# Optimization experiments

Measured on AMD Instinct MI355X. Metric: run time of the kernel, lower is better.

Reference implementation:

```python
import jax, jax.numpy as jnp
import numpy as np

FEATURE_DIM = 6272
UNITS = 32
B, L = 8, 256

def setup_inputs() -> dict:
    key = jax.random.key(0)
    k1, k2, k3, k4, k5 = jax.random.split(key, 5)
    return {
        "inputs": jax.random.normal(k1, (B, L, FEATURE_DIM), dtype=jnp.float32),
        "Wt": jax.random.normal(k2, (FEATURE_DIM, UNITS), dtype=jnp.float32) * 0.02,
        "bh": jax.random.normal(k3, (UNITS,), dtype=jnp.float32),
        "Wa": jax.random.normal(k4, (UNITS, 1), dtype=jnp.float32) * 0.02,
        "ba": jax.random.normal(k5, (1,), dtype=jnp.float32),
    }

def reference(inputs, Wt, bh, Wa, ba):
    # q == k: both projected through Wt (original code reuses Wt for both)
    p = jnp.einsum('blf,fu->blu', inputs, Wt)            # [B, L, U]
    # additive (Bahdanau-style) pairwise combine: [B, L, L, U]
    beta = jnp.tanh(p[:, :, None, :] + p[:, None, :, :] + bh)
    alpha = jnp.einsum('bqku,uo->bqk', beta, Wa) + ba[0]  # [B, L, L]
    alpha = jax.nn.sigmoid(alpha)
    a = jax.nn.softmax(alpha, axis=-1)                    # softmax over keys
    c_r = jnp.einsum('bqk,bkf->bqf', a, inputs)           # [B, L, F]
    return c_r
```

## Files before the change

### kernel.cpp

```cpp
#include <hip/hip_runtime.h>
#include <hip/hip_bf16.h>
#include <math.h>

#define FDIM 6272
#define LQ   256
#define BN   8
#define UDIM 32
#define BL   (BN*LQ)

typedef short  short8 __attribute__((ext_vector_type(8)));
typedef float  f32x4  __attribute__((ext_vector_type(4)));

static __device__ __forceinline__ ushort f2bf(float f) {
    __hip_bfloat16 h = __float2bfloat16(f);
    return *(ushort*)&h;
}

__global__ __launch_bounds__(256)
void k_wtt(const float* __restrict__ Wt, ushort* __restrict__ wtt,
           float* __restrict__ pb) {
    const int gid = blockIdx.x * 256 + threadIdx.x;
    const int u = gid / 784, fg = gid % 784;
    ushort v[8];
    #pragma unroll
    for (int j = 0; j < 8; ++j)
        v[j] = f2bf(Wt[(size_t)(8 * fg + j) * UDIM + u]);
    *(uint4*)(wtt + (size_t)u * FDIM + 8 * fg) = *(uint4*)v;

    if (gid < BL * UDIM / 4)
        ((float4*)pb)[gid] = make_float4(0.f, 0.f, 0.f, 0.f);
}

__global__ __launch_bounds__(256)
void k1_mfma(const float* __restrict__ x, const ushort* __restrict__ wtt,
             float* __restrict__ pb) {
    __shared__ ushort As[32 * 40];
    __shared__ ushort Bs[32 * 40];

    const int t    = threadIdx.x;
    const int row0 = blockIdx.x * 32;
    const int f0   = blockIdx.y * 896;
    const int wv   = t >> 6, lane = t & 63;
    const int n16  = lane & 15, quad = lane >> 4;
    const int m0   = 16 * (wv & 1), n0 = 16 * (wv >> 1);

    const int srow = t >> 3, sg = t & 7;

    f32x4 acc = (f32x4){0.f, 0.f, 0.f, 0.f};

    for (int c = 0; c < 28; ++c) {
        const int kk = f0 + c * 32;
        __syncthreads();
        const float4 xv = *(const float4*)(x + (size_t)(row0 + srow) * FDIM + kk + 4 * sg);
        uint2 pk;
        pk.x = (unsigned)f2bf(xv.x) | ((unsigned)f2bf(xv.y) << 16);
        pk.y = (unsigned)f2bf(xv.z) | ((unsigned)f2bf(xv.w) << 16);
        *(uint2*)(As + srow * 40 + 4 * sg) = pk;
        *(uint2*)(Bs + srow * 40 + 4 * sg) =
            *(const uint2*)(wtt + (size_t)srow * FDIM + kk + 4 * sg);
        __syncthreads();

        const short8 af = *(const short8*)(As + (m0 + n16) * 40 + quad * 8);
        const short8 bf = *(const short8*)(Bs + (n0 + n16) * 40 + quad * 8);
        acc = __builtin_amdgcn_mfma_f32_16x16x32_bf16(af, bf, acc, 0, 0, 0);
    }

    #pragma unroll
    for (int r = 0; r < 4; ++r)
        atomicAdd(&pb[(size_t)(row0 + m0 + quad * 4 + r) * UDIM + n0 + n16], acc[r]);
}

__global__ __launch_bounds__(256)
void k2_attn(const float* __restrict__ pb, const float* __restrict__ bh,
             const float* __restrict__ Wa, const float* __restrict__ ba,
             ushort* __restrict__ ab) {
    const int bq = blockIdx.x;
    const int b  = bq >> 8;
    const int k  = threadIdx.x;

    __shared__ float pq_s[UDIM];
    __shared__ float wa_s[UDIM];
    __shared__ float pk_s[LQ * 33];
    __shared__ float red[4];

    if (k < UDIM) {
        pq_s[k] = pb[bq * UDIM + k] + bh[k];
        wa_s[k] = Wa[k];
    }
    const float* pbb = pb + (size_t)b * LQ * UDIM;
    #pragma unroll
    for (int i = 0; i < 32; ++i) {
        int idx = k + i * 256;
        pk_s[(idx >> 5) * 33 + (idx & 31)] = pbb[idx];
    }
    __syncthreads();

    const float* pk = &pk_s[k * 33];
    float s = 0.f;
    #pragma unroll
    for (int u = 0; u < UDIM; ++u)
        s = fmaf(tanhf(pq_s[u] + pk[u]), wa_s[u], s);

    const float alpha = 1.f / (1.f + expf(-(s + ba[0])));
    const float e = expf(alpha);

    float v = e;
    #pragma unroll
    for (int m = 1; m < 64; m <<= 1) v += __shfl_xor(v, m, 64);
    if ((k & 63) == 0) red[k >> 6] = v;
    __syncthreads();
    const float tot = red[0] + red[1] + red[2] + red[3];

    ab[(size_t)bq * LQ + k] = f2bf(e / tot);
}

__global__ __launch_bounds__(256, 3)
void k3_fused(const float* __restrict__ x, const ushort* __restrict__ ab,
              float* __restrict__ out) {
    __shared__ ushort Bs[64 * 40];

    const int t    = threadIdx.x;
    const int f0   = blockIdx.x * 64;
    const int b    = blockIdx.y;
    const int wv   = t >> 6;
    const int lane = t & 63;
    const int n16  = lane & 15;
    const int quad = lane >> 4;

    const int g  = t >> 4;
    const int kp = t & 15;

    const float*  xb  = x  + (size_t)b * LQ * FDIM + f0 + 4 * g;
    const ushort* abb = ab + (size_t)b * LQ * LQ;

    f32x4 acc[4][4];
    #pragma unroll
    for (int mf = 0; mf < 4; ++mf)
        #pragma unroll
        for (int nf = 0; nf < 4; ++nf)
            acc[mf][nf] = (f32x4){0.f, 0.f, 0.f, 0.f};

    for (int c = 0; c < 8; ++c) {
        const int kc = c * 32;
        __syncthreads();
        {
            const float4 v0 = *(const float4*)(xb + (size_t)(kc + 2 * kp    ) * FDIM);
            const float4 v1 = *(const float4*)(xb + (size_t)(kc + 2 * kp + 1) * FDIM);
            unsigned* bw = (unsigned*)Bs;
            bw[(4 * g + 0) * 20 + kp] = (unsigned)f2bf(v0.x) | ((unsigned)f2bf(v1.x) << 16);
            bw[(4 * g + 1) * 20 + kp] = (unsigned)f2bf(v0.y) | ((unsigned)f2bf(v1.y) << 16);
            bw[(4 * g + 2) * 20 + kp] = (unsigned)f2bf(v0.z) | ((unsigned)f2bf(v1.z) << 16);
            bw[(4 * g + 3) * 20 + kp] = (unsigned)f2bf(v0.w) | ((unsigned)f2bf(v1.w) << 16);
        }
        __syncthreads();

        short8 af[4];
        #pragma unroll
        for (int mf = 0; mf < 4; ++mf)
            af[mf] = *(const short8*)(abb + (size_t)(64 * wv + 16 * mf + n16) * LQ
                                      + kc + quad * 8);
        #pragma unroll
        for (int nf = 0; nf < 4; ++nf) {
            const short8 bf = *(const short8*)(Bs + (16 * nf + n16) * 40 + quad * 8);
            #pragma unroll
            for (int mf = 0; mf < 4; ++mf)
                acc[mf][nf] = __builtin_amdgcn_mfma_f32_16x16x32_bf16(af[mf], bf, acc[mf][nf], 0, 0, 0);
        }
    }

    float* ob = out + ((size_t)b * LQ + 64 * wv + quad * 4) * FDIM + f0 + n16;
    #pragma unroll
    for (int mf = 0; mf < 4; ++mf)
        #pragma unroll
        for (int nf = 0; nf < 4; ++nf)
            #pragma unroll
            for (int r = 0; r < 4; ++r)
                ob[(size_t)(16 * mf + r) * FDIM + 16 * nf] = acc[mf][nf][r];
}

extern "C" void kernel_launch(void* const* d_in, const int* in_sizes, int n_in,
                              void* d_out, int out_size, void* d_ws, size_t ws_size,
                              hipStream_t stream) {
    const float* x  = (const float*)d_in[0];
    const float* Wt = (const float*)d_in[1];
    const float* bh = (const float*)d_in[2];
    const float* Wa = (const float*)d_in[3];
    const float* ba = (const float*)d_in[4];
    float* out = (float*)d_out;

    float*  pb  = (float*)d_ws;
    ushort* ab  = (ushort*)((char*)d_ws + 262144);
    ushort* wtt = (ushort*)((char*)d_ws + 262144 + 1048576);

    k_wtt<<<98, 256, 0, stream>>>(Wt, wtt, pb);
    k1_mfma<<<dim3(64, 7), 256, 0, stream>>>(x, wtt, pb);
    k2_attn<<<BL, 256, 0, stream>>>(pb, bh, Wa, ba, ab);
    k3_fused<<<dim3(98, 8), 256, 0, stream>>>(x, ab, out);
}
```

Measured before the change: 168.5 us.

## Double-buffer k3 LDS tiles, drop LDS staging in k1, use fast math in k2

k3 now stages 64-deep K chunks into two LDS buffers, prefetching the next chunk's x into registers while the current chunk's MFMAs run. This halves the number of barriers and hides global load latency. k1 drops its shared-memory staging and loads MFMA fragments straight from global memory with an unrolled loop. k2 replaces tanhf, expf and division with raw v_exp/v_rcp approximations, which slightly reduces accuracy. k3 also loses its occupancy hint, and the larger LDS and register footprint may lower occupancy.

```diff
diff --git a/kernel.cpp b/kernel.cpp
--- a/kernel.cpp
+++ b/kernel.cpp
@@ -15,6 +15,22 @@
     __hip_bfloat16 h = __float2bfloat16(f);
     return *(ushort*)&h;
 }
+static __device__ __forceinline__ unsigned pk2(float a, float b) {
+    return (unsigned)f2bf(a) | ((unsigned)f2bf(b) << 16);
+}
+static __device__ __forceinline__ float fexp2(float x) {
+    float r;
+    asm volatile("v_exp_f32 %0, %1 \n s_nop 1" : "=v"(r) : "v"(x));
+    return r;
+}
+static __device__ __forceinline__ float frcp(float x) {
+    float r;
+    asm volatile("v_rcp_f32 %0, %1 \n s_nop 1" : "=v"(r) : "v"(x));
+    return r;
+}
+static __device__ __forceinline__ float tanh_fast(float v) {
+    return 1.f - 2.f * frcp(1.f + fexp2(v * 2.88539008177793f));
+}
 
 __global__ __launch_bounds__(256)
 void k_wtt(const float* __restrict__ Wt, ushort* __restrict__ wtt,
@@ -34,40 +50,34 @@
 __global__ __launch_bounds__(256)
 void k1_mfma(const float* __restrict__ x, const ushort* __restrict__ wtt,
              float* __restrict__ pb) {
-    __shared__ ushort As[32 * 40];
-    __shared__ ushort Bs[32 * 40];
-
     const int t    = threadIdx.x;
-    const int row0 = blockIdx.x * 32;
-    const int f0   = blockIdx.y * 896;
     const int wv   = t >> 6, lane = t & 63;
     const int n16  = lane & 15, quad = lane >> 4;
-    const int m0   = 16 * (wv & 1), n0 = 16 * (wv >> 1);
-
-    const int srow = t >> 3, sg = t & 7;
+    const int row0 = blockIdx.x * 32 + 16 * (wv & 1);
+    const int u0   = 16 * (wv >> 1);
+    const int f0   = blockIdx.y * 896;
+
+    const float*  xr = x   + (size_t)(row0 + n16) * FDIM + f0 + quad * 8;
+    const ushort* wr = wtt + (size_t)(u0   + n16) * FDIM + f0 + quad * 8;
 
     f32x4 acc = (f32x4){0.f, 0.f, 0.f, 0.f};
 
+    #pragma unroll 4
     for (int c = 0; c < 28; ++c) {
-        const int kk = f0 + c * 32;
-        __syncthreads();
-        const float4 xv = *(const float4*)(x + (size_t)(row0 + srow) * FDIM + kk + 4 * sg);
-        uint2 pk;
-        pk.x = (unsigned)f2bf(xv.x) | ((unsigned)f2bf(xv.y) << 16);
-        pk.y = (unsigned)f2bf(xv.z) | ((unsigned)f2bf(xv.w) << 16);
-        *(uint2*)(As + srow * 40 + 4 * sg) = pk;
-        *(uint2*)(Bs + srow * 40 + 4 * sg) =
-            *(const uint2*)(wtt + (size_t)srow * FDIM + kk + 4 * sg);
-        __syncthreads();
-
-        const short8 af = *(const short8*)(As + (m0 + n16) * 40 + quad * 8);
-        const short8 bf = *(const short8*)(Bs + (n0 + n16) * 40 + quad * 8);
+        const float4 a0 = *(const float4*)(xr + c * 32);
+        const float4 a1 = *(const float4*)(xr + c * 32 + 4);
+        short8 af;
+        af[0] = (short)f2bf(a0.x); af[1] = (short)f2bf(a0.y);
+        af[2] = (short)f2bf(a0.z); af[3] = (short)f2bf(a0.w);
+        af[4] = (short)f2bf(a1.x); af[5] = (short)f2bf(a1.y);
+        af[6] = (short)f2bf(a1.z); af[7] = (short)f2bf(a1.w);
+        const short8 bf = *(const short8*)(wr + c * 32);
         acc = __builtin_amdgcn_mfma_f32_16x16x32_bf16(af, bf, acc, 0, 0, 0);
     }
 
     #pragma unroll
     for (int r = 0; r < 4; ++r)
-        atomicAdd(&pb[(size_t)(row0 + m0 + quad * 4 + r) * UDIM + n0 + n16], acc[r]);
+        atomicAdd(&pb[(size_t)(row0 + quad * 4 + r) * UDIM + u0 + n16], acc[r]);
 }
 
 __global__ __launch_bounds__(256)
@@ -75,18 +85,15 @@
              const float* __restrict__ Wa, const float* __restrict__ ba,
              ushort* __restrict__ ab) {
     const int bq = blockIdx.x;
-    const int b  = bq >> 8;
+    const int b  = bq >> 8, q = bq & 255;
     const int k  = threadIdx.x;
 
+    __shared__ float pk_s[LQ * 33];
     __shared__ float pq_s[UDIM];
     __shared__ float wa_s[UDIM];
-    __shared__ float pk_s[LQ * 33];
     __shared__ float red[4];
 
-    if (k < UDIM) {
-        pq_s[k] = pb[bq * UDIM + k] + bh[k];
-        wa_s[k] = Wa[k];
-    }
+    if (k < UDIM) wa_s[k] = Wa[k];
     const float* pbb = pb + (size_t)b * LQ * UDIM;
     #pragma unroll
     for (int i = 0; i < 32; ++i) {
@@ -94,15 +101,17 @@
         pk_s[(idx >> 5) * 33 + (idx & 31)] = pbb[idx];
     }
     __syncthreads();
+    if (k < UDIM) pq_s[k] = pk_s[q * 33 + k] + bh[k];
+    __syncthreads();
 
     const float* pk = &pk_s[k * 33];
     float s = 0.f;
     #pragma unroll
     for (int u = 0; u < UDIM; ++u)
-        s = fmaf(tanhf(pq_s[u] + pk[u]), wa_s[u], s);
-
-    const float alpha = 1.f / (1.f + expf(-(s + ba[0])));
-    const float e = expf(alpha);
+        s = fmaf(tanh_fast(pq_s[u] + pk[u]), wa_s[u], s);
+
+    const float alpha = frcp(1.f + fexp2(-(s + ba[0]) * 1.44269504088896f));
+    const float e = fexp2(alpha * 1.44269504088896f);
 
     float v = e;
     #pragma unroll
@@ -111,13 +120,13 @@
     __syncthreads();
     const float tot = red[0] + red[1] + red[2] + red[3];
 
-    ab[(size_t)bq * LQ + k] = f2bf(e / tot);
-}
-
-__global__ __launch_bounds__(256, 3)
+    ab[(size_t)bq * LQ + k] = f2bf(e * frcp(tot));
+}
+
+__global__ __launch_bounds__(256)
 void k3_fused(const float* __restrict__ x, const ushort* __restrict__ ab,
               float* __restrict__ out) {
-    __shared__ ushort Bs[64 * 40];
+    __shared__ ushort Bs[2][64 * 72];
 
     const int t    = threadIdx.x;
     const int f0   = blockIdx.x * 64;
@@ -126,9 +135,8 @@
     const int lane = t & 63;
     const int n16  = lane & 15;
     const int quad = lane >> 4;
-
-    const int g  = t >> 4;
-    const int kp = t & 15;
+    const int g    = t >> 4;
+    const int kp   = t & 15;
 
     const float*  xb  = x  + (size_t)b * LQ * FDIM + f0 + 4 * g;
     const ushort* abb = ab + (size_t)b * LQ * LQ;
@@ -140,33 +148,55 @@
         for (int nf = 0; nf < 4; ++nf)
             acc[mf][nf] = (f32x4){0.f, 0.f, 0.f, 0.f};
 
-    for (int c = 0; c < 8; ++c) {
-        const int kc = c * 32;
+    float4 pv0, pv1, pv2, pv3;
+#define LDX(kc) do {                                                   \
+        pv0 = *(const float4*)(xb + (size_t)((kc) + 2 * kp     ) * FDIM); \
+        pv1 = *(const float4*)(xb + (size_t)((kc) + 2 * kp +  1) * FDIM); \
+        pv2 = *(const float4*)(xb + (size_t)((kc) + 2 * kp + 32) * FDIM); \
+        pv3 = *(const float4*)(xb + (size_t)((kc) + 2 * kp + 33) * FDIM); \
+    } while (0)
+#define STX(bufi) do {                                                 \
+        unsigned* bw = (unsigned*)(Bs[bufi]);                          \
+        bw[(4 * g + 0) * 36 + kp]      = pk2(pv0.x, pv1.x);            \
+        bw[(4 * g + 1) * 36 + kp]      = pk2(pv0.y, pv1.y);            \
+        bw[(4 * g + 2) * 36 + kp]      = pk2(pv0.z, pv1.z);            \
+        bw[(4 * g + 3) * 36 + kp]      = pk2(pv0.w, pv1.w);            \
+        bw[(4 * g + 0) * 36 + kp + 16] = pk2(pv2.x, pv3.x);            \
+        bw[(4 * g + 1) * 36 + kp + 16] = pk2(pv2.y, pv3.y);            \
+        bw[(4 * g + 2) * 36 + kp + 16] = pk2(pv2.z, pv3.z);            \
+        bw[(4 * g + 3) * 36 + kp + 16] = pk2(pv2.w, pv3.w);            \
+    } while (0)
+
+    LDX(0);
+    STX(0);
+
+    for (int c = 0; c < 4; ++c) {
+        if (c < 3) LDX((c + 1) * 64);
+        short8 af[4][2];
+        #pragma unroll
+        for (int mf = 0; mf < 4; ++mf)
+            #pragma unroll
+            for (int h = 0; h < 2; ++h)
+                af[mf][h] = *(const short8*)(abb
+                    + (size_t)(64 * wv + 16 * mf + n16) * LQ
+                    + c * 64 + h * 32 + quad * 8);
         __syncthreads();
-        {
-            const float4 v0 = *(const float4*)(xb + (size_t)(kc + 2 * kp    ) * FDIM);
-            const float4 v1 = *(const float4*)(xb + (size_t)(kc + 2 * kp + 1) * FDIM);
-            unsigned* bw = (unsigned*)Bs;
-            bw[(4 * g + 0) * 20 + kp] = (unsigned)f2bf(v0.x) | ((unsigned)f2bf(v1.x) << 16);
-            bw[(4 * g + 1) * 20 + kp] = (unsigned)f2bf(v0.y) | ((unsigned)f2bf(v1.y) << 16);
-            bw[(4 * g + 2) * 20 + kp] = (unsigned)f2bf(v0.z) | ((unsigned)f2bf(v1.z) << 16);
-            bw[(4 * g + 3) * 20 + kp] = (unsigned)f2bf(v0.w) | ((unsigned)f2bf(v1.w) << 16);
-        }
-        __syncthreads();
-
-        short8 af[4];
-        #pragma unroll
-        for (int mf = 0; mf < 4; ++mf)
-            af[mf] = *(const short8*)(abb + (size_t)(64 * wv + 16 * mf + n16) * LQ
-                                      + kc + quad * 8);
-        #pragma unroll
-        for (int nf = 0; nf < 4; ++nf) {
-            const short8 bf = *(const short8*)(Bs + (16 * nf + n16) * 40 + quad * 8);
+        const ushort* bsc = Bs[c & 1];
+        #pragma unroll
+        for (int h = 0; h < 2; ++h)
             #pragma unroll
-            for (int mf = 0; mf < 4; ++mf)
-                acc[mf][nf] = __builtin_amdgcn_mfma_f32_16x16x32_bf16(af[mf], bf, acc[mf][nf], 0, 0, 0);
-        }
+            for (int nf = 0; nf < 4; ++nf) {
+                const short8 bf = *(const short8*)(bsc + (16 * nf + n16) * 72
+                                                   + h * 32 + quad * 8);
+                #pragma unroll
+                for (int mf = 0; mf < 4; ++mf)
+                    acc[mf][nf] = __builtin_amdgcn_mfma_f32_16x16x32_bf16(
+                        af[mf][h], bf, acc[mf][nf], 0, 0, 0);
+            }
+        if (c < 3) STX((c + 1) & 1);
     }
+#undef LDX
+#undef STX
 
     float* ob = out + ((size_t)b * LQ + 64 * wv + quad * 4) * FDIM + f0 + n16;
     #pragma unroll
```

Measured after the change: 163.7 us. 2.9% less time.
